# Kernel tuning notes

Measured on AMD Instinct MI355X. Metric: run time of the kernel, lower is better.

## Reference

```python
import jax, jax.numpy as jnp
import numpy as np

NEG_BIG = -1e4  # matches torch masked_fill(-1e4)


def word_average(hidden, word_ids, num_words):
    """Segment-mean of token embeddings into word embeddings.
    hidden: [M, L, D], word_ids: [M, L] int in [0, num_words).
    Returns (word_reprs [M, W, D], word_mask [M, W] bool).
    Equivalent to average_by_spans: each word repr is the mean of its subword tokens;
    words with no tokens (the torch code's skipped [-1] spans) get a zero repr and mask=0.
    """
    M, L, D = hidden.shape
    seg = (jnp.arange(M, dtype=word_ids.dtype)[:, None] * num_words + word_ids).reshape(-1)
    sums = jax.ops.segment_sum(hidden.reshape(M * L, D), seg, num_segments=M * num_words)
    counts = jax.ops.segment_sum(jnp.ones((M * L,), hidden.dtype), seg, num_segments=M * num_words)
    sums = sums.reshape(M, num_words, D)
    counts = counts.reshape(M, num_words)
    mask = counts > 0
    reprs = sums / jnp.maximum(counts, 1.0)[..., None]
    return reprs, mask


def scope_pool(word_reprs, mask, proj_w, proj_b, scope_importance):
    """scope_proj_head (eval-mode dropout = identity) + scope_aware_pooling.
    word_reprs: [M, W, D], mask: [M, W]. Returns (pooled [M, D], logits [M, W, S]).
    Logits at invalid (padded) word slots are zeroed, matching torch pad_sequence padding
    applied after the projection.
    """
    logits = (jnp.einsum('mwd,ds->mws', word_reprs, proj_w) + proj_b) * mask[..., None].astype(word_reprs.dtype)
    scope_probs = jax.nn.softmax(logits, axis=-1)                      # [M, W, S]
    importance = jnp.einsum('mws,s->mw', scope_probs, scope_importance)
    importance = jnp.where(mask, importance, NEG_BIG)
    weights = jax.nn.softmax(importance, axis=-1)                      # [M, W]
    pooled = jnp.einsum('mw,mwd->md', weights, word_reprs)             # [M, D]
    return pooled, logits


def setup_inputs() -> dict:
    key = jax.random.key(0)
    ks = jax.random.split(key, 9)
    B, N, Lq, Lp, D, S = 16, 7, 256, 512, 768, 12
    Wq, Wp = 200, 400
    return {
        'q_hidden': jax.random.normal(ks[0], (B, Lq, D), jnp.float32),
        'pos_hidden': jax.random.normal(ks[1], (B, Lp, D), jnp.float32),
        'neg_hidden': jax.random.normal(ks[2], (B, N, Lp, D), jnp.float32),
        'proj_w': jax.random.normal(ks[3], (D, S), jnp.float32) * 0.02,
        'proj_b': jax.random.normal(ks[4], (S,), jnp.float32) * 0.02,
        'scope_importance': jax.random.uniform(ks[5], (S,), jnp.float32),
        'q_word_ids': jax.random.randint(ks[6], (B, Lq), 0, Wq, jnp.int32),
        'pos_word_ids': jax.random.randint(ks[7], (B, Lp), 0, Wp, jnp.int32),
        'neg_word_ids': jax.random.randint(ks[8], (B, N, Lp), 0, Wp, jnp.int32),
    }


def reference(q_hidden, pos_hidden, neg_hidden, proj_w, proj_b, scope_importance,
              q_word_ids, pos_word_ids, neg_word_ids):
    Wq = 200
    Wp = 400
    B, N, Lp, D = neg_hidden.shape

    # per-sample span averaging (ragged segment means)
    q_word, q_mask = word_average(q_hidden, q_word_ids, Wq)
    p_word, p_mask = word_average(pos_hidden, pos_word_ids, Wp)
    n_word, n_mask = word_average(neg_hidden.reshape(B * N, Lp, D),
                                  neg_word_ids.reshape(B * N, Lp), Wp)

    # scope projection + scope-aware softmax pooling
    q_pooled, q_logits = scope_pool(q_word, q_mask, proj_w, proj_b, scope_importance)
    p_pooled, p_logits = scope_pool(p_word, p_mask, proj_w, proj_b, scope_importance)
    n_pooled, _ = scope_pool(n_word, n_mask, proj_w, proj_b, scope_importance)
    n_pooled = n_pooled.reshape(B, N, D)

    return q_pooled, p_pooled, q_logits, p_logits, n_pooled
```

## Files before the change

### kernel.cpp

```cpp
#include <hip/hip_runtime.h>
#include <cfloat>

#define NEG_BIG (-1e4f)

constexpr int D = 768;
constexpr int S = 12;

constexpr int Lq = 256, Lp = 512, Wq = 200, Wp = 400;
constexpr int Mq = 16, Mp = 16, Mn = 112;

constexpr int OFF_WSUM_Q = 0;
constexpr int OFF_WSUM_P = 38400;
constexpr int OFF_WSUM_N = 115200;
constexpr int OFF_CNT_Q  = 652800;
constexpr int OFF_CNT_P  = 656000;
constexpr int OFF_CNT_N  = 662400;
constexpr int OFF_IMP_Q  = 707200;
constexpr int OFF_IMP_P  = 710400;
constexpr int OFF_IMP_N  = 716800;
constexpr int OFF_COEF   = 761600;
constexpr int WS_ZERO_FLOATS = 707200;

constexpr int OUT_QP = 0;
constexpr int OUT_PP = 12288;
constexpr int OUT_QL = 24576;
constexpr int OUT_PL = 62976;
constexpr int OUT_NP = 139776;

__global__ __launch_bounds__(64) void k_proj_accum(
    const float* __restrict__ q_h, const float* __restrict__ p_h,
    const float* __restrict__ n_h, const int* __restrict__ q_ids,
    const int* __restrict__ p_ids, const int* __restrict__ n_ids,
    const float* __restrict__ pw, float* __restrict__ ws)
{
    const int bx   = blockIdx.x;
    const int lane = threadIdx.x;

    const float* h; const int* ids; float* wsum; float* cnt;
    int W, Lshift, tile, half;
    if (bx < 128)      { h = q_h; ids = q_ids; wsum = ws + OFF_WSUM_Q; cnt = ws + OFF_CNT_Q;
                         W = Wq; Lshift = 8; tile = bx >> 1; half = bx & 1; }
    else if (bx < 384) { int r = bx - 128;
                         h = p_h; ids = p_ids; wsum = ws + OFF_WSUM_P; cnt = ws + OFF_CNT_P;
                         W = Wp; Lshift = 9; tile = r >> 1; half = r & 1; }
    else               { int r = bx - 384;
                         h = n_h; ids = n_ids; wsum = ws + OFF_WSUM_N; cnt = ws + OFF_CNT_N;
                         W = Wp; Lshift = 9; tile = r >> 1; half = r & 1; }

    const int flat = tile * 64 + lane;
    const int m    = flat >> Lshift;
    const int id   = ids[flat];

    const int d0 = half * 384;
    const float* hrow  = h + (size_t)flat * D + d0;
    const float* wbase = pw + (size_t)d0 * S;

    float p[S];
#pragma unroll
    for (int s = 0; s < S; ++s) p[s] = 0.f;

#pragma unroll 4
    for (int dg = 0; dg < 96; ++dg) {
        const float4 hv = *(const float4*)(hrow + 4 * dg);
        const float* wr = wbase + (size_t)dg * 48;
        const float hj[4] = {hv.x, hv.y, hv.z, hv.w};
#pragma unroll
        for (int j = 0; j < 4; ++j)
#pragma unroll
            for (int s = 0; s < S; ++s)
                p[s] = fmaf(hj[j], wr[12 * j + s], p[s]);
    }

    float* wb = wsum + ((size_t)m * W + id) * S;
#pragma unroll
    for (int s = 0; s < S; ++s) atomicAdd(wb + s, p[s]);
    if (half == 0) atomicAdd(cnt + (size_t)m * W + id, 1.0f);
}

__global__ void k_finalize(
    const float* __restrict__ ws_c, float* __restrict__ ws_mut,
    const float* __restrict__ pb, const float* __restrict__ simp,
    float* __restrict__ out)
{
    const int idx = blockIdx.x * blockDim.x + threadIdx.x;
    if (idx >= Mq * Wq + Mp * Wp + Mn * Wp) return;

    const float* wsum; float c; float* imp; float* lgout;
    if (idx < Mq * Wq) {
        wsum = ws_c + OFF_WSUM_Q + (size_t)idx * S;  c = ws_c[OFF_CNT_Q + idx];
        imp = ws_mut + OFF_IMP_Q + idx;              lgout = out + OUT_QL + (size_t)idx * S;
    } else if (idx < Mq * Wq + Mp * Wp) {
        const int r = idx - Mq * Wq;
        wsum = ws_c + OFF_WSUM_P + (size_t)r * S;    c = ws_c[OFF_CNT_P + r];
        imp = ws_mut + OFF_IMP_P + r;                lgout = out + OUT_PL + (size_t)r * S;
    } else {
        const int r = idx - Mq * Wq - Mp * Wp;
        wsum = ws_c + OFF_WSUM_N + (size_t)r * S;    c = ws_c[OFF_CNT_N + r];
        imp = ws_mut + OFF_IMP_N + r;                lgout = nullptr;
    }

    const bool valid = (c > 0.5f);
    const float inv = valid ? 1.0f / c : 0.0f;

    float lg[S];
#pragma unroll
    for (int s = 0; s < S; ++s)
        lg[s] = valid ? (wsum[s] * inv + pb[s]) : 0.0f;

    float mx = lg[0];
#pragma unroll
    for (int s = 1; s < S; ++s) mx = fmaxf(mx, lg[s]);
    float sum = 0.f, acc = 0.f;
#pragma unroll
    for (int s = 0; s < S; ++s) {
        float e = expf(lg[s] - mx);
        sum += e;
        acc += e * simp[s];
    }
    *imp = valid ? (acc / sum) : NEG_BIG;

    if (lgout) {
#pragma unroll
        for (int s = 0; s < S; ++s) lgout[s] = lg[s];
    }
}

__global__ __launch_bounds__(256) void k_coef(
    const int* __restrict__ q_ids, const int* __restrict__ p_ids,
    const int* __restrict__ n_ids, float* __restrict__ ws)
{
    __shared__ float s_red[256];
    __shared__ float s_wgt[Wp];

    const int by  = blockIdx.x;
    const int tid = threadIdx.x;

    const int* ids; const float* impm; const float* cntm; int L, W;
    if (by < Mq)           { int m = by;
        ids = q_ids + m * Lq; impm = ws + OFF_IMP_Q + m * Wq;
        cntm = ws + OFF_CNT_Q + m * Wq; L = Lq; W = Wq; }
    else if (by < Mq + Mp) { int m = by - Mq;
        ids = p_ids + m * Lp; impm = ws + OFF_IMP_P + m * Wp;
        cntm = ws + OFF_CNT_P + m * Wp; L = Lp; W = Wp; }
    else                   { int m = by - Mq - Mp;
        ids = n_ids + m * Lp; impm = ws + OFF_IMP_N + m * Wp;
        cntm = ws + OFF_CNT_N + m * Wp; L = Lp; W = Wp; }
    float* coef = ws + OFF_COEF + (size_t)by * 512;

    float lm = -FLT_MAX;
    for (int w = tid; w < W; w += 256) lm = fmaxf(lm, impm[w]);
    s_red[tid] = lm;
    __syncthreads();
    for (int st = 128; st > 0; st >>= 1) {
        if (tid < st) s_red[tid] = fmaxf(s_red[tid], s_red[tid + st]);
        __syncthreads();
    }
    const float mx = s_red[0];
    __syncthreads();

    float ls = 0.f;
    for (int w = tid; w < W; w += 256) {
        float e = expf(impm[w] - mx);
        s_wgt[w] = e;
        ls += e;
    }
    s_red[tid] = ls;
    __syncthreads();
    for (int st = 128; st > 0; st >>= 1) {
        if (tid < st) s_red[tid] += s_red[tid + st];
        __syncthreads();
    }
    const float inv = 1.0f / s_red[0];
    for (int w = tid; w < W; w += 256) s_wgt[w] *= inv;
    __syncthreads();

    for (int l = tid; l < L; l += 256) {
        const int id = ids[l];
        coef[l] = s_wgt[id] / cntm[id];
    }
}

__global__ __launch_bounds__(192) void k_pool(
    const float* __restrict__ q_h, const float* __restrict__ p_h,
    const float* __restrict__ n_h, const float* __restrict__ ws,
    float* __restrict__ out)
{
    __shared__ float s_c[64];

    const int bx  = blockIdx.x;
    const int tid = threadIdx.x;

    const float* h; float* outp; int L, m, t0, cby;
    if (bx < 64)       { m = bx >> 2;  t0 = (bx & 3) * 64;
        h = q_h; outp = out + OUT_QP + (size_t)m * D; L = Lq; cby = m; }
    else if (bx < 192) { int r = bx - 64;  m = r >> 3;  t0 = (r & 7) * 64;
        h = p_h; outp = out + OUT_PP + (size_t)m * D; L = Lp; cby = Mq + m; }
    else               { int r = bx - 192; m = r >> 3;  t0 = (r & 7) * 64;
        h = n_h; outp = out + OUT_NP + (size_t)m * D; L = Lp; cby = Mq + Mp + m; }

    if (tid < 64) s_c[tid] = ws[OFF_COEF + (size_t)cby * 512 + t0 + tid];
    __syncthreads();

    const float* hb = h + (size_t)m * L * D + (size_t)t0 * D + 4 * tid;

    float4 acc = make_float4(0.f, 0.f, 0.f, 0.f);
#pragma unroll 8
    for (int l = 0; l < 64; ++l) {
        const float4 hv = *(const float4*)(hb + (size_t)l * D);
        const float c = s_c[l];
        acc.x = fmaf(c, hv.x, acc.x);
        acc.y = fmaf(c, hv.y, acc.y);
        acc.z = fmaf(c, hv.z, acc.z);
        acc.w = fmaf(c, hv.w, acc.w);
    }

    float* op = outp + 4 * tid;
    atomicAdd(op + 0, acc.x);
    atomicAdd(op + 1, acc.y);
    atomicAdd(op + 2, acc.z);
    atomicAdd(op + 3, acc.w);
}

extern "C" void kernel_launch(void* const* d_in, const int* in_sizes, int n_in,
                              void* d_out, int out_size, void* d_ws, size_t ws_size,
                              hipStream_t stream)
{
    const float* q_hidden   = (const float*)d_in[0];
    const float* pos_hidden = (const float*)d_in[1];
    const float* neg_hidden = (const float*)d_in[2];
    const float* proj_w     = (const float*)d_in[3];
    const float* proj_b     = (const float*)d_in[4];
    const float* simp       = (const float*)d_in[5];
    const int*   q_ids      = (const int*)d_in[6];
    const int*   p_ids      = (const int*)d_in[7];
    const int*   n_ids      = (const int*)d_in[8];
    float* out = (float*)d_out;
    float* ws  = (float*)d_ws;

    hipMemsetAsync(d_ws, 0, (size_t)WS_ZERO_FLOATS * sizeof(float), stream);
    hipMemsetAsync(out, 0, (size_t)24576 * sizeof(float), stream);
    hipMemsetAsync(out + OUT_NP, 0, (size_t)(Mn * D) * sizeof(float), stream);

    k_proj_accum<<<dim3(2176), dim3(64), 0, stream>>>(
        q_hidden, pos_hidden, neg_hidden, q_ids, p_ids, n_ids, proj_w, ws);

    k_finalize<<<dim3((Mq * Wq + Mp * Wp + Mn * Wp + 255) / 256), dim3(256), 0, stream>>>(
        ws, ws, proj_b, simp, out);

    k_coef<<<dim3(Mq + Mp + Mn), dim3(256), 0, stream>>>(q_ids, p_ids, n_ids, ws);

    k_pool<<<dim3(1088), dim3(192), 0, stream>>>(
        q_hidden, pos_hidden, neg_hidden, ws, out);
}
```

Baseline: 419.7 us.

## Stage hidden rows through swizzled LDS for coalesced loads in projection kernel

The projection-accumulate kernel now uses 256-thread blocks with four independent waves. Each wave cooperatively loads 8-row by 32-column tiles of hidden states with coalesced float4 reads into an XOR-swizzled LDS buffer, then each lane reads back its own token row. The next tile is register-prefetched while the current one is consumed. This replaces the per-lane strided row reads, which were poorly coalesced, at the cost of LDS traffic and extra registers.

Result: slower. 465.1 us (+10.8%).

```diff
diff --git a/kernel.cpp b/kernel.cpp
--- a/kernel.cpp
+++ b/kernel.cpp
@@ -27,48 +27,76 @@
 constexpr int OUT_PL = 62976;
 constexpr int OUT_NP = 139776;
 
-__global__ __launch_bounds__(64) void k_proj_accum(
+__global__ __launch_bounds__(256) void k_proj_accum(
     const float* __restrict__ q_h, const float* __restrict__ p_h,
     const float* __restrict__ n_h, const int* __restrict__ q_ids,
     const int* __restrict__ p_ids, const int* __restrict__ n_ids,
     const float* __restrict__ pw, float* __restrict__ ws)
 {
+    __shared__ float lds[4 * 2048];
+
     const int bx   = blockIdx.x;
-    const int lane = threadIdx.x;
+    const int lane = threadIdx.x & 63;
+    const int wv   = threadIdx.x >> 6;
+
+    const int half = bx & 1;
+    const int d0   = half * 384;
+    const int tidg = (bx >> 1) * 4 + wv;
 
     const float* h; const int* ids; float* wsum; float* cnt;
-    int W, Lshift, tile, half;
-    if (bx < 128)      { h = q_h; ids = q_ids; wsum = ws + OFF_WSUM_Q; cnt = ws + OFF_CNT_Q;
-                         W = Wq; Lshift = 8; tile = bx >> 1; half = bx & 1; }
-    else if (bx < 384) { int r = bx - 128;
-                         h = p_h; ids = p_ids; wsum = ws + OFF_WSUM_P; cnt = ws + OFF_CNT_P;
-                         W = Wp; Lshift = 9; tile = r >> 1; half = r & 1; }
-    else               { int r = bx - 384;
-                         h = n_h; ids = n_ids; wsum = ws + OFF_WSUM_N; cnt = ws + OFF_CNT_N;
-                         W = Wp; Lshift = 9; tile = r >> 1; half = r & 1; }
-
-    const int flat = tile * 64 + lane;
-    const int m    = flat >> Lshift;
-    const int id   = ids[flat];
-
-    const int d0 = half * 384;
-    const float* hrow  = h + (size_t)flat * D + d0;
-    const float* wbase = pw + (size_t)d0 * S;
+    int W, Lshift, tile;
+    if (tidg < 64)       { h = q_h; ids = q_ids; wsum = ws + OFF_WSUM_Q; cnt = ws + OFF_CNT_Q;
+                           W = Wq; Lshift = 8; tile = tidg; }
+    else if (tidg < 192) { h = p_h; ids = p_ids; wsum = ws + OFF_WSUM_P; cnt = ws + OFF_CNT_P;
+                           W = Wp; Lshift = 9; tile = tidg - 64; }
+    else                 { h = n_h; ids = n_ids; wsum = ws + OFF_WSUM_N; cnt = ws + OFF_CNT_N;
+                           W = Wp; Lshift = 9; tile = tidg - 192; }
+
+    const int flat0 = tile * 64;
+    const int token = flat0 + lane;
+    const int m     = token >> Lshift;
+    const int id    = ids[token];
+
+    float* wlds = lds + wv * 2048;
+
+    const int srow   = lane >> 3;
+    const int schunk = lane & 7;
+    const int dslot  = schunk ^ srow;
+    const float* gbase = h + (size_t)(flat0 + srow) * D + d0 + schunk * 4;
+    float*       lwb   = wlds + srow * 32 + dslot * 4;
 
     float p[S];
 #pragma unroll
     for (int s = 0; s < S; ++s) p[s] = 0.f;
 
-#pragma unroll 4
-    for (int dg = 0; dg < 96; ++dg) {
-        const float4 hv = *(const float4*)(hrow + 4 * dg);
-        const float* wr = wbase + (size_t)dg * 48;
-        const float hj[4] = {hv.x, hv.y, hv.z, hv.w};
-#pragma unroll
-        for (int j = 0; j < 4; ++j)
-#pragma unroll
-            for (int s = 0; s < S; ++s)
-                p[s] = fmaf(hj[j], wr[12 * j + s], p[s]);
+    float4 rg[8];
+#pragma unroll
+    for (int i = 0; i < 8; ++i)
+        rg[i] = *(const float4*)(gbase + (size_t)(8 * i) * D);
+
+    for (int dt = 0; dt < 12; ++dt) {
+#pragma unroll
+        for (int i = 0; i < 8; ++i)
+            *(float4*)(lwb + i * 256) = rg[i];
+
+        if (dt + 1 < 12) {
+#pragma unroll
+            for (int i = 0; i < 8; ++i)
+                rg[i] = *(const float4*)(gbase + (size_t)(8 * i) * D + (dt + 1) * 32);
+        }
+
+        const float* wt = pw + (size_t)(d0 + dt * 32) * S;
+#pragma unroll
+        for (int c = 0; c < 8; ++c) {
+            const float4 hv = *(const float4*)(wlds + lane * 32 + ((c ^ (lane & 7)) * 4));
+            const float* wr = wt + c * 48;
+            const float hj[4] = {hv.x, hv.y, hv.z, hv.w};
+#pragma unroll
+            for (int j = 0; j < 4; ++j)
+#pragma unroll
+                for (int s = 0; s < S; ++s)
+                    p[s] = fmaf(hj[j], wr[j * 12 + s], p[s]);
+        }
     }
 
     float* wb = wsum + ((size_t)m * W + id) * S;
@@ -241,7 +269,7 @@
     hipMemsetAsync(out, 0, (size_t)24576 * sizeof(float), stream);
     hipMemsetAsync(out + OUT_NP, 0, (size_t)(Mn * D) * sizeof(float), stream);
 
-    k_proj_accum<<<dim3(2176), dim3(64), 0, stream>>>(
+    k_proj_accum<<<dim3(544), dim3(256), 0, stream>>>(
         q_hidden, pos_hidden, neg_hidden, q_ids, p_ids, n_ids, proj_w, ws);
 
     k_finalize<<<dim3((Mq * Wq + Mp * Wp + Mn * Wp + 255) / 256), dim3(256), 0, stream>>>(
```
